# Optimization experiments

Measured on AMD Instinct MI355X. Metric: run time of the kernel, lower is better.

Reference implementation:

```python
import math
import jax, jax.numpy as jnp
import numpy as np

B, S, D = 2, 2048, 1024
N_HEADS, D_KV = 16, 64
INNER = N_HEADS * D_KV
NUM_BUCKETS = 32
MAX_DISTANCE = 128


def _relative_position_bucket(relative_position, num_buckets=NUM_BUCKETS, max_distance=MAX_DISTANCE):
    # bidirectional (encoder) variant
    nb = num_buckets // 2
    rel_buckets = (relative_position > 0).astype(jnp.int32) * nb
    rp = jnp.abs(relative_position)
    max_exact = nb // 2
    is_small = rp < max_exact
    rp_safe = jnp.maximum(rp, 1)  # avoid log(0); selected away by where
    rp_if_large = max_exact + (
        jnp.log(rp_safe.astype(jnp.float32) / max_exact)
        / math.log(max_distance / max_exact)
        * (nb - max_exact)
    ).astype(jnp.int32)
    rp_if_large = jnp.minimum(rp_if_large, nb - 1)
    return rel_buckets + jnp.where(is_small, rp, rp_if_large)


def compute_bias(rel_bias, q_len, k_len):
    ctx = jnp.arange(q_len)[:, None]
    mem = jnp.arange(k_len)[None, :]
    buckets = _relative_position_bucket(mem - ctx)  # [q_len, k_len]
    values = rel_bias[buckets]                      # [q_len, k_len, H]
    return jnp.transpose(values, (2, 0, 1))[None]   # [1, H, q_len, k_len]


def setup_inputs() -> dict:
    key = jax.random.key(0)
    ks = jax.random.split(key, 6)
    s = 1.0 / math.sqrt(D)
    return {
        "hidden_states": jax.random.normal(ks[0], (B, S, D), jnp.float32),
        "wq": jax.random.normal(ks[1], (D, INNER), jnp.float32) * s,
        "wk": jax.random.normal(ks[2], (D, INNER), jnp.float32) * s,
        "wv": jax.random.normal(ks[3], (D, INNER), jnp.float32) * s,
        "wo": jax.random.normal(ks[4], (INNER, D), jnp.float32) * s,
        "rel_bias": jax.random.normal(ks[5], (NUM_BUCKETS, N_HEADS), jnp.float32) * 0.1,
    }


def reference(hidden_states, wq, wk, wv, wo, rel_bias):
    b, s, _ = hidden_states.shape

    def shape(x):  # [b, s, inner] -> [b, h, s, d_kv]
        return x.reshape(b, s, N_HEADS, D_KV).transpose(0, 2, 1, 3)

    q = shape(hidden_states @ wq)  # note: T5 has NO 1/sqrt(d) scaling
    k = shape(hidden_states @ wk)
    v = shape(hidden_states @ wv)

    scores = jnp.einsum("bhqd,bhkd->bhqk", q, k)
    position_bias = compute_bias(rel_bias, s, s)
    scores = scores + position_bias
    attn = jax.nn.softmax(scores.astype(jnp.float32), axis=-1).astype(scores.dtype)

    out = jnp.einsum("bhqk,bhkd->bhqd", attn, v)
    out = out.transpose(0, 2, 1, 3).reshape(b, s, INNER)
    return out @ wo
```

## Files before the change

kernel.cpp:

```cpp
#include <hip/hip_runtime.h>
#include <hip/hip_bf16.h>

#define B_ 2
#define S_ 2048
#define D_ 1024
#define H_ 16
#define DKV_ 64
#define INNER_ 1024
#define M_ (B_*S_)

typedef unsigned short ushort_t;
typedef unsigned int u32;
typedef __bf16 bf16x8 __attribute__((ext_vector_type(8)));
typedef __bf16 bf16x4 __attribute__((ext_vector_type(4)));
typedef float f32x4 __attribute__((ext_vector_type(4)));

#define VMCNT0 asm volatile("s_waitcnt vmcnt(0)" ::: "memory")
#define LOG2E 1.4426950408889634f

__device__ __forceinline__ unsigned short f2bf(float f) {
    unsigned int u = __builtin_bit_cast(unsigned int, f);
    unsigned int r = (u + 0x7fffu + ((u >> 16) & 1u)) >> 16;
    return (unsigned short)r;
}

__device__ __forceinline__ void gload16(const ushort_t* g, ushort_t* l) {
    __builtin_amdgcn_global_load_lds(
        (const __attribute__((address_space(1))) u32*)g,
        (__attribute__((address_space(3))) u32*)l, 16, 0, 0);
}

__global__ __launch_bounds__(256) void prep_kernel(
        const float* __restrict__ hs,
        const float* __restrict__ s0, const float* __restrict__ s1,
        const float* __restrict__ s2, const float* __restrict__ s3,
        const float* __restrict__ rb,
        unsigned short* __restrict__ Abf,
        unsigned short* __restrict__ d0, unsigned short* __restrict__ d1,
        unsigned short* __restrict__ d2, unsigned short* __restrict__ d3,
        float* __restrict__ btab) {
    int bid = blockIdx.x, tid = threadIdx.x;
    if (bid < 4096) {
        int i = (bid * 256 + tid) * 4;
        float4 v = *(const float4*)&hs[i];
        ushort4 o;
        o.x = f2bf(v.x); o.y = f2bf(v.y); o.z = f2bf(v.z); o.w = f2bf(v.w);
        *(ushort4*)&Abf[i] = o;
    } else if (bid < 5120) {
        int t = bid - 4096;
        int z = t >> 8, rem = t & 255;
        int k0 = ((rem >> 4) & 15) * 64, n0 = (rem & 15) * 64;
        const float* srcs[4] = {s0, s1, s2, s3};
        unsigned short* dsts[4] = {d0, d1, d2, d3};
        const float* src = srcs[z];
        unsigned short* dst = dsts[z];
        __shared__ float tbuf[64][65];
        for (int i = tid; i < 4096; i += 256) {
            int r = i >> 6, c = i & 63;
            tbuf[r][c] = src[(k0 + r) * 1024 + n0 + c];
        }
        __syncthreads();
        for (int i = tid; i < 4096; i += 256) {
            int r = i >> 6, c = i & 63;
            dst[(n0 + r) * 1024 + k0 + c] = f2bf(tbuf[c][r]);
        }
    } else {
        #pragma unroll
        for (int j = 0; j < 4; ++j) {
            int idx = (bid - 5120) * 1024 + j * 256 + tid;
            int h = idx >> 12, pos = idx & 4095;
            int rel = pos - 2048;
            int bb = rel > 0 ? 16 : 0;
            int rp = rel < 0 ? -rel : rel;
            int bucket;
            if (rp < 8) bucket = bb + rp;
            else {
                int v = 8 + (int)(logf((float)rp * 0.125f) / 2.7725887f * 8.0f);
                bucket = bb + (v < 15 ? v : 15);
            }
            btab[idx] = rb[bucket * 16 + h] * LOG2E;
        }
    }
}

__global__ __launch_bounds__(256) void gemm_qkv(const ushort_t* __restrict__ A,
        const ushort_t* __restrict__ WQ, const ushort_t* __restrict__ WK, const ushort_t* __restrict__ WV,
        ushort_t* __restrict__ Qb, ushort_t* __restrict__ Kb, ushort_t* __restrict__ Vtb) {
    __shared__ alignas(16) ushort_t As[128][64];
    __shared__ alignas(16) ushort_t Bs[128][64];
    int tid = threadIdx.x, wid = tid >> 6, lane = tid & 63;
    int linear = blockIdx.x;
    int swz = (linear & 7) * 96 + (linear >> 3);
    int m0 = (swz / 24) * 128;
    int nblk = swz % 24;
    int sel = nblk >> 3;
    const ushort_t* Bt = sel == 0 ? WQ : (sel == 1 ? WK : WV);
    int n0 = (nblk & 7) * 128;
    int lr = lane & 15, lg = lane >> 4;
    int wm = (wid >> 1) * 64, wn = (wid & 1) * 64;
    int srow = tid >> 3, sp = tid & 7;
    int scol = (sp ^ (srow & 7)) * 8;
    int cR0 = (lg ^ (lr & 7)) * 8;
    int cR1 = ((4 + lg) ^ (lr & 7)) * 8;
    const ushort_t* Abase = A + (size_t)m0 * 1024 + scol;
    const ushort_t* Bbase = Bt + (size_t)n0 * 1024 + scol;
    f32x4 acc[4][4] = {};
    for (int kt = 0; kt < 1024; kt += 64) {
        #pragma unroll
        for (int j = 0; j < 4; ++j) {
            int row = j * 32 + srow;
            gload16(Abase + row * 1024 + kt, &As[0][0] + (j * 256 + tid) * 8);
            gload16(Bbase + row * 1024 + kt, &Bs[0][0] + (j * 256 + tid) * 8);
        }
        VMCNT0;
        __syncthreads();
        bf16x8 af[4][2], bfr[4][2];
        #pragma unroll
        for (int t = 0; t < 4; ++t) {
            af[t][0]  = *(const bf16x8*)&As[wm + t * 16 + lr][cR0];
            af[t][1]  = *(const bf16x8*)&As[wm + t * 16 + lr][cR1];
            bfr[t][0] = *(const bf16x8*)&Bs[wn + t * 16 + lr][cR0];
            bfr[t][1] = *(const bf16x8*)&Bs[wn + t * 16 + lr][cR1];
        }
        #pragma unroll
        for (int hh = 0; hh < 2; ++hh)
            #pragma unroll
            for (int i2 = 0; i2 < 4; ++i2)
                #pragma unroll
                for (int j2 = 0; j2 < 4; ++j2)
                    acc[i2][j2] = __builtin_amdgcn_mfma_f32_16x16x32_bf16(af[i2][hh], bfr[j2][hh], acc[i2][j2], 0, 0, 0);
        __syncthreads();
    }
    #pragma unroll
    for (int i2 = 0; i2 < 4; ++i2)
        #pragma unroll
        for (int j2 = 0; j2 < 4; ++j2) {
            int col = n0 + wn + j2 * 16 + lr;
            int hh = col >> 6, d = col & 63;
            if (sel < 2) {
                ushort_t* dst = sel == 0 ? Qb : Kb;
                #pragma unroll
                for (int r = 0; r < 4; ++r) {
                    int row = m0 + wm + i2 * 16 + lg * 4 + r;
                    int b = row >> 11, s = row & 2047;
                    dst[(((size_t)(b * H_ + hh) * S_ + s)) * DKV_ + d] = f2bf(acc[i2][j2][r]);
                }
            } else {
                int row0 = m0 + wm + i2 * 16 + lg * 4;
                int b = row0 >> 11, s0 = row0 & 2047;
                ushort4 sv;
                sv.x = f2bf(acc[i2][j2][0]); sv.y = f2bf(acc[i2][j2][1]);
                sv.z = f2bf(acc[i2][j2][2]); sv.w = f2bf(acc[i2][j2][3]);
                *(ushort4*)&Vtb[((size_t)(b * H_ + hh) * DKV_ + d) * S_ + s0] = sv;
            }
        }
}

__global__ __launch_bounds__(256) void gemm_out(const ushort_t* __restrict__ A,
                                                const ushort_t* __restrict__ Bt,
                                                float* __restrict__ C) {
    __shared__ alignas(16) ushort_t As[64][64];
    __shared__ alignas(16) ushort_t Bs[128][64];
    int tid = threadIdx.x, wid = tid >> 6, lane = tid & 63;
    int linear = blockIdx.x;
    int swz = (linear & 7) * 64 + (linear >> 3);
    int m0 = (swz >> 3) * 64, n0 = (swz & 7) * 128;
    int lr = lane & 15, lg = lane >> 4;
    int wn = wid * 32;
    int srow = tid >> 3, sp = tid & 7;
    int scol = (sp ^ (srow & 7)) * 8;
    int cR0 = (lg ^ (lr & 7)) * 8;
    int cR1 = ((4 + lg) ^ (lr & 7)) * 8;
    const ushort_t* Abase = A + (size_t)m0 * 1024 + scol;
    const ushort_t* Bbase = Bt + (size_t)n0 * 1024 + scol;
    f32x4 acc[4][2] = {};
    for (int kt = 0; kt < 1024; kt += 64) {
        #pragma unroll
        for (int j = 0; j < 2; ++j) {
            int row = j * 32 + srow;
            gload16(Abase + row * 1024 + kt, &As[0][0] + (j * 256 + tid) * 8);
        }
        #pragma unroll
        for (int j = 0; j < 4; ++j) {
            int row = j * 32 + srow;
            gload16(Bbase + row * 1024 + kt, &Bs[0][0] + (j * 256 + tid) * 8);
        }
        VMCNT0;
        __syncthreads();
        bf16x8 af[4][2], bfr[2][2];
        #pragma unroll
        for (int t = 0; t < 4; ++t) {
            af[t][0] = *(const bf16x8*)&As[t * 16 + lr][cR0];
            af[t][1] = *(const bf16x8*)&As[t * 16 + lr][cR1];
        }
        #pragma unroll
        for (int j = 0; j < 2; ++j) {
            bfr[j][0] = *(const bf16x8*)&Bs[wn + j * 16 + lr][cR0];
            bfr[j][1] = *(const bf16x8*)&Bs[wn + j * 16 + lr][cR1];
        }
        #pragma unroll
        for (int hh = 0; hh < 2; ++hh)
            #pragma unroll
            for (int i2 = 0; i2 < 4; ++i2)
                #pragma unroll
                for (int j2 = 0; j2 < 2; ++j2)
                    acc[i2][j2] = __builtin_amdgcn_mfma_f32_16x16x32_bf16(af[i2][hh], bfr[j2][hh], acc[i2][j2], 0, 0, 0);
        __syncthreads();
    }
    #pragma unroll
    for (int i2 = 0; i2 < 4; ++i2)
        #pragma unroll
        for (int j2 = 0; j2 < 2; ++j2)
            #pragma unroll
            for (int r = 0; r < 4; ++r)
                C[(size_t)(m0 + i2 * 16 + lg * 4 + r) * 1024 + n0 + wn + j2 * 16 + lr] = acc[i2][j2][r];
}

__global__ __launch_bounds__(256, 2) void flash_attn(const ushort_t* __restrict__ Q,
                                                     const ushort_t* __restrict__ Kg,
                                                     const ushort_t* __restrict__ Vt,
                                                     const float* __restrict__ bias_tab,
                                                     ushort_t* __restrict__ Out) {
    __shared__ alignas(16) ushort_t Ks[3][64][64];
    __shared__ alignas(16) ushort_t Ps[4][16][64];
    __shared__ float LbS[2176];
    int tid = threadIdx.x, wid = tid >> 6, lane = tid & 63;
    int linear = blockIdx.x;
    int swz = (linear & 7) * 64 + (linear >> 3);
    int bh = swz >> 4, qblk = swz & 15;
    int h = bh & 15, b = bh >> 4;
    int q0b = qblk * 128;
    int q0w = q0b + wid * 32;
    int lr = lane & 15, lg = lane >> 4;

    {
        const float* bsrc = bias_tab + h * 4096 + 2048 - q0b - 127;
        for (int i = tid; i < 2175; i += 256) LbS[i] = bsrc[i];
    }
    float cpos = bias_tab[h * 4096 + 4095];
    float cneg = bias_tab[h * 4096 + 0];

    const ushort_t* Qbase = Q + ((size_t)bh * S_ + q0w) * DKV_;
    bf16x8 qA0 = *(const bf16x8*)&Qbase[lr * DKV_ + lg * 8];
    bf16x8 qA1 = *(const bf16x8*)&Qbase[lr * DKV_ + 32 + lg * 8];
    bf16x8 qB0 = *(const bf16x8*)&Qbase[(16 + lr) * DKV_ + lg * 8];
    bf16x8 qB1 = *(const bf16x8*)&Qbase[(16 + lr) * DKV_ + 32 + lg * 8];

    int srow = tid >> 3, sp = tid & 7;
    int kc = (sp ^ (srow & 7)) * 8;
    const ushort_t* Ksrc = Kg + (size_t)bh * S_ * DKV_ + kc;
    const ushort_t* Vfrag = Vt + ((size_t)bh * DKV_ + lr) * S_ + lg * 8;
    int c0 = (lg ^ (lr & 7)) * 8;
    int c1 = ((4 + lg) ^ (lr & 7)) * 8;
    int pxor = (lr & 7) << 4;

    f32x4 oA[4] = {}, oB[4] = {};
    f32x4 lpA = {}, lpB = {};
    const int bbA = 127 - wid * 32 + 4 * lg - lr;
    const int bbB = bbA - 16;

    auto stageK = [&](int bi, int kt) {
        ushort_t* kb = &Ks[bi][0][0];
        gload16(Ksrc + (size_t)(kt + srow) * 64,      kb + tid * 8);
        gload16(Ksrc + (size_t)(kt + 32 + srow) * 64, kb + 2048 + tid * 8);
    };
    auto loadV = [&](int kt, bf16x8 (&v)[4][2]) {
        #pragma unroll
        for (int dt = 0; dt < 4; ++dt) {
            const ushort_t* vp = Vfrag + (size_t)dt * 16 * S_ + kt;
            v[dt][0] = *(const bf16x8*)vp;
            v[dt][1] = *(const bf16x8*)(vp + 32);
        }
    };
    auto qk = [&](int buf, f32x4* sA, f32x4* sB) {
        __builtin_amdgcn_s_setprio(1);
        #pragma unroll
        for (int nt = 0; nt < 4; ++nt) {
            bf16x8 kf0 = *(const bf16x8*)&Ks[buf][nt * 16 + lr][c0];
            bf16x8 kf1 = *(const bf16x8*)&Ks[buf][nt * 16 + lr][c1];
            sA[nt] = __builtin_amdgcn_mfma_f32_16x16x32_bf16(kf0, qA0, sA[nt], 0, 0, 0);
            sA[nt] = __builtin_amdgcn_mfma_f32_16x16x32_bf16(kf1, qA1, sA[nt], 0, 0, 0);
            sB[nt] = __builtin_amdgcn_mfma_f32_16x16x32_bf16(kf0, qB0, sB[nt], 0, 0, 0);
            sB[nt] = __builtin_amdgcn_mfma_f32_16x16x32_bf16(kf1, qB1, sB[nt], 0, 0, 0);
        }
        __builtin_amdgcn_s_setprio(0);
    };
    auto smpv = [&](f32x4 (&s)[4], f32x4& lp, f32x4 (&o)[4],
                    int bi, bool far, float cb, const bf16x8 (&vf)[4][2]) {
        float p[4][4];
        if (far) {
            #pragma unroll
            for (int nt = 0; nt < 4; ++nt)
                #pragma unroll
                for (int r = 0; r < 4; ++r)
                    p[nt][r] = __builtin_amdgcn_exp2f(fmaf(s[nt][r], LOG2E, cb));
        } else {
            #pragma unroll
            for (int nt = 0; nt < 4; ++nt)
                #pragma unroll
                for (int r = 0; r < 4; ++r)
                    p[nt][r] = __builtin_amdgcn_exp2f(fmaf(s[nt][r], LOG2E, LbS[bi + nt * 16 + r]));
        }
        char* pbase = (char*)&Ps[wid][lr][0];
        #pragma unroll
        for (int nt = 0; nt < 4; ++nt) {
            #pragma unroll
            for (int r = 0; r < 4; ++r) lp[r] += p[nt][r];
            bf16x4 pv;
            pv[0] = (__bf16)p[nt][0]; pv[1] = (__bf16)p[nt][1];
            pv[2] = (__bf16)p[nt][2]; pv[3] = (__bf16)p[nt][3];
            *(bf16x4*)(pbase + ((nt * 32 + lg * 8) ^ pxor)) = pv;
        }
        bf16x8 pf0 = *(const bf16x8*)(pbase + ((lg * 16) ^ pxor));
        bf16x8 pf1 = *(const bf16x8*)(pbase + ((64 + lg * 16) ^ pxor));
        __builtin_amdgcn_s_setprio(1);
        #pragma unroll
        for (int dt = 0; dt < 4; ++dt) {
            o[dt] = __builtin_amdgcn_mfma_f32_16x16x32_bf16(vf[dt][0], pf0, o[dt], 0, 0, 0);
            o[dt] = __builtin_amdgcn_mfma_f32_16x16x32_bf16(vf[dt][1], pf1, o[dt], 0, 0, 0);
        }
        __builtin_amdgcn_s_setprio(0);
    };

    bf16x8 vu[4][2], vn[4][2];
    f32x4 sCA[4] = {}, sCB[4] = {};

    stageK(0, 0);
    stageK(1, 64);
    stageK(2, 128);
    loadV(0, vu);
    asm volatile("s_waitcnt vmcnt(10) lgkmcnt(0)" ::: "memory");
    __builtin_amdgcn_s_barrier();
    __builtin_amdgcn_sched_barrier(0);
    qk(0, sCA, sCB);
    __builtin_amdgcn_s_barrier();
    __builtin_amdgcn_sched_barrier(0);

    #pragma unroll 2
    for (int t = 0; t < 32; ++t) {
        const int kt = t * 64;
        const bool even = (t & 1) == 0;
        bf16x8 (&vuse)[4][2] = even ? vu : vn;
        bf16x8 (&vnxt)[4][2] = even ? vn : vu;
        if (t <= 28) stageK(t % 3, kt + 192);
        if (t < 31) loadV(kt + 64, vnxt);
        __builtin_amdgcn_sched_barrier(0);
        f32x4 sNA[4] = {}, sNB[4] = {};
        if (t < 31) {
            int nb = (t + 1) % 3;
            qk(nb, sNA, sNB);
        }
        const bool far = (kt >= q0b + 256) || (kt + 64 <= q0b - 128);
        const float cb = (kt > q0b) ? cpos : cneg;
        smpv(sCA, lpA, oA, kt + bbA, far, cb, vuse);
        smpv(sCB, lpB, oB, kt + bbB, far, cb, vuse);
        #pragma unroll
        for (int nt = 0; nt < 4; ++nt) { sCA[nt] = sNA[nt]; sCB[nt] = sNB[nt]; }
        if (t < 31) {
            if (t <= 28) { asm volatile("s_waitcnt vmcnt(10)" ::: "memory"); }
            else         { asm volatile("s_waitcnt vmcnt(8)"  ::: "memory"); }
            __builtin_amdgcn_s_barrier();
            __builtin_amdgcn_sched_barrier(0);
        }
    }

    float lA = (lpA[0] + lpA[1]) + (lpA[2] + lpA[3]);
    lA += __shfl_xor(lA, 16); lA += __shfl_xor(lA, 32);
    float lB = (lpB[0] + lpB[1]) + (lpB[2] + lpB[3]);
    lB += __shfl_xor(lB, 16); lB += __shfl_xor(lB, 32);
    {
        float linv = 1.f / lA;
        char* pbase = (char*)&Ps[wid][lr][0];
        #pragma unroll
        for (int dt = 0; dt < 4; ++dt) {
            bf16x4 ov;
            ov[0] = (__bf16)(oA[dt][0] * linv); ov[1] = (__bf16)(oA[dt][1] * linv);
            ov[2] = (__bf16)(oA[dt][2] * linv); ov[3] = (__bf16)(oA[dt][3] * linv);
            *(bf16x4*)(pbase + ((dt * 32 + lg * 8) ^ pxor)) = ov;
        }
        int row = lane >> 2, seg = lane & 3;
        int rxor = (row & 7) << 4;
        char* rbase = (char*)&Ps[wid][row][0];
        uint4 v0 = *(uint4*)(rbase + ((seg * 32) ^ rxor));
        uint4 v1 = *(uint4*)(rbase + ((seg * 32 + 16) ^ rxor));
        ushort_t* dst = Out + (size_t)(b * S_ + q0w + row) * INNER_ + h * DKV_ + seg * 16;
        *(uint4*)&dst[0] = v0;
        *(uint4*)&dst[8] = v1;
    }
    {
        float linv = 1.f / lB;
        char* pbase = (char*)&Ps[wid][lr][0];
        #pragma unroll
        for (int dt = 0; dt < 4; ++dt) {
            bf16x4 ov;
            ov[0] = (__bf16)(oB[dt][0] * linv); ov[1] = (__bf16)(oB[dt][1] * linv);
            ov[2] = (__bf16)(oB[dt][2] * linv); ov[3] = (__bf16)(oB[dt][3] * linv);
            *(bf16x4*)(pbase + ((dt * 32 + lg * 8) ^ pxor)) = ov;
        }
        int row = lane >> 2, seg = lane & 3;
        int rxor = (row & 7) << 4;
        char* rbase = (char*)&Ps[wid][row][0];
        uint4 v0 = *(uint4*)(rbase + ((seg * 32) ^ rxor));
        uint4 v1 = *(uint4*)(rbase + ((seg * 32 + 16) ^ rxor));
        ushort_t* dst = Out + (size_t)(b * S_ + q0w + 16 + row) * INNER_ + h * DKV_ + seg * 16;
        *(uint4*)&dst[0] = v0;
        *(uint4*)&dst[8] = v1;
    }
}

extern "C" void kernel_launch(void* const* d_in, const int* in_sizes, int n_in,
                              void* d_out, int out_size, void* d_ws, size_t ws_size,
                              hipStream_t stream) {
    const float* hs = (const float*)d_in[0];
    const float* wq = (const float*)d_in[1];
    const float* wk = (const float*)d_in[2];
    const float* wv = (const float*)d_in[3];
    const float* wo = (const float*)d_in[4];
    const float* rb = (const float*)d_in[5];

    char* ws = (char*)d_ws;
    unsigned short* Abf = (unsigned short*)(ws);
    unsigned short* Wqt = (unsigned short*)(ws + (8u  << 20));
    unsigned short* Wkt = (unsigned short*)(ws + (10u << 20));
    unsigned short* Wvt = (unsigned short*)(ws + (12u << 20));
    unsigned short* Wot = (unsigned short*)(ws + (14u << 20));
    unsigned short* Qb  = (unsigned short*)(ws + (16u << 20));
    unsigned short* Kb  = (unsigned short*)(ws + (24u << 20));
    unsigned short* Vtb = (unsigned short*)(ws + (32u << 20));
    unsigned short* AOb = (unsigned short*)(ws + (40u << 20));
    float*          Btab = (float*)(ws + (48u << 20));

    prep_kernel<<<5184, 256, 0, stream>>>(hs, wq, wk, wv, wo, rb,
                                          Abf, Wqt, Wkt, Wvt, Wot, Btab);

    gemm_qkv<<<768, 256, 0, stream>>>(Abf, Wqt, Wkt, Wvt, Qb, Kb, Vtb);

    flash_attn<<<512, 256, 0, stream>>>(Qb, Kb, Vtb, Btab, AOb);

    gemm_out<<<512, 256, 0, stream>>>(AOb, Wot, (float*)d_out);
}
```

Baseline: 133.7 us.

## Feed P to PV MFMA directly from registers via 16x16x16 bf16 instruction

Replaces the LDS round-trip for the softmax probabilities (write P to shared memory, read back in K=32 layout) with the 16x16x16 bf16 MFMA, whose B-operand layout matches the QK accumulator layout, so P feeds the PV product straight from registers. V fragments are reloaded as 4-element chunks (16 narrower loads per tile instead of 8), and the vmcnt waits are adjusted to match. This removes LDS writes and reads plus their latency per tile, at the cost of twice as many MFMA issues for PV and more, smaller global loads. The old path is kept as a fallback when the builtin is unavailable.

```diff
diff --git a/kernel.cpp b/kernel.cpp
--- a/kernel.cpp
+++ b/kernel.cpp
@@ -13,6 +13,7 @@
 typedef unsigned int u32;
 typedef __bf16 bf16x8 __attribute__((ext_vector_type(8)));
 typedef __bf16 bf16x4 __attribute__((ext_vector_type(4)));
+typedef short s16x4 __attribute__((ext_vector_type(4)));
 typedef float f32x4 __attribute__((ext_vector_type(4)));
 
 #define VMCNT0 asm volatile("s_waitcnt vmcnt(0)" ::: "memory")
@@ -29,6 +30,14 @@
         (const __attribute__((address_space(1))) u32*)g,
         (__attribute__((address_space(3))) u32*)l, 16, 0, 0);
 }
+
+#if __has_builtin(__builtin_amdgcn_mfma_f32_16x16x16bf16_1k)
+#define HAVE_MFMA16 1
+__device__ __forceinline__ f32x4 mfma16(bf16x4 a, bf16x4 b, f32x4 c) {
+    return __builtin_amdgcn_mfma_f32_16x16x16bf16_1k(
+        __builtin_bit_cast(s16x4, a), __builtin_bit_cast(s16x4, b), c, 0, 0, 0);
+}
+#endif
 
 __global__ __launch_bounds__(256) void prep_kernel(
         const float* __restrict__ hs,
@@ -216,6 +225,7 @@
                 C[(size_t)(m0 + i2 * 16 + lg * 4 + r) * 1024 + n0 + wn + j2 * 16 + lr] = acc[i2][j2][r];
 }
 
+#ifdef HAVE_MFMA16
 __global__ __launch_bounds__(256, 2) void flash_attn(const ushort_t* __restrict__ Q,
                                                      const ushort_t* __restrict__ Kg,
                                                      const ushort_t* __restrict__ Vt,
@@ -249,7 +259,7 @@
     int srow = tid >> 3, sp = tid & 7;
     int kc = (sp ^ (srow & 7)) * 8;
     const ushort_t* Ksrc = Kg + (size_t)bh * S_ * DKV_ + kc;
-    const ushort_t* Vfrag = Vt + ((size_t)bh * DKV_ + lr) * S_ + lg * 8;
+    const ushort_t* VfragB = Vt + ((size_t)bh * DKV_ + lr) * S_ + lg * 4;
     int c0 = (lg ^ (lr & 7)) * 8;
     int c1 = ((4 + lg) ^ (lr & 7)) * 8;
     int pxor = (lr & 7) << 4;
@@ -264,13 +274,12 @@
         gload16(Ksrc + (size_t)(kt + srow) * 64,      kb + tid * 8);
         gload16(Ksrc + (size_t)(kt + 32 + srow) * 64, kb + 2048 + tid * 8);
     };
-    auto loadV = [&](int kt, bf16x8 (&v)[4][2]) {
-        #pragma unroll
-        for (int dt = 0; dt < 4; ++dt) {
-            const ushort_t* vp = Vfrag + (size_t)dt * 16 * S_ + kt;
-            v[dt][0] = *(const bf16x8*)vp;
-            v[dt][1] = *(const bf16x8*)(vp + 32);
-        }
+    auto loadV = [&](int kt, bf16x4 (&v)[4][4]) {
+        #pragma unroll
+        for (int dt = 0; dt < 4; ++dt)
+            #pragma unroll
+            for (int nt = 0; nt < 4; ++nt)
+                v[dt][nt] = *(const bf16x4*)(VfragB + (size_t)dt * 16 * S_ + kt + nt * 16);
     };
     auto qk = [&](int buf, f32x4* sA, f32x4* sB) {
         __builtin_amdgcn_s_setprio(1);
@@ -286,7 +295,7 @@
         __builtin_amdgcn_s_setprio(0);
     };
     auto smpv = [&](f32x4 (&s)[4], f32x4& lp, f32x4 (&o)[4],
-                    int bi, bool far, float cb, const bf16x8 (&vf)[4][2]) {
+                    int bi, bool far, float cb, const bf16x4 (&vf)[4][4]) {
         float p[4][4];
         if (far) {
             #pragma unroll
@@ -301,6 +310,189 @@
                 for (int r = 0; r < 4; ++r)
                     p[nt][r] = __builtin_amdgcn_exp2f(fmaf(s[nt][r], LOG2E, LbS[bi + nt * 16 + r]));
         }
+        bf16x4 pk[4];
+        #pragma unroll
+        for (int nt = 0; nt < 4; ++nt) {
+            #pragma unroll
+            for (int r = 0; r < 4; ++r) lp[r] += p[nt][r];
+            pk[nt][0] = (__bf16)p[nt][0]; pk[nt][1] = (__bf16)p[nt][1];
+            pk[nt][2] = (__bf16)p[nt][2]; pk[nt][3] = (__bf16)p[nt][3];
+        }
+        __builtin_amdgcn_s_setprio(1);
+        #pragma unroll
+        for (int dt = 0; dt < 4; ++dt)
+            #pragma unroll
+            for (int nt = 0; nt < 4; ++nt)
+                o[dt] = mfma16(vf[dt][nt], pk[nt], o[dt]);
+        __builtin_amdgcn_s_setprio(0);
+    };
+
+    bf16x4 vu[4][4], vn[4][4];
+    f32x4 sCA[4] = {}, sCB[4] = {};
+
+    stageK(0, 0);
+    stageK(1, 64);
+    stageK(2, 128);
+    loadV(0, vu);
+    asm volatile("s_waitcnt vmcnt(18) lgkmcnt(0)" ::: "memory");
+    __builtin_amdgcn_s_barrier();
+    __builtin_amdgcn_sched_barrier(0);
+    qk(0, sCA, sCB);
+    __builtin_amdgcn_s_barrier();
+    __builtin_amdgcn_sched_barrier(0);
+
+    #pragma unroll 2
+    for (int t = 0; t < 32; ++t) {
+        const int kt = t * 64;
+        const bool even = (t & 1) == 0;
+        bf16x4 (&vuse)[4][4] = even ? vu : vn;
+        bf16x4 (&vnxt)[4][4] = even ? vn : vu;
+        if (t <= 28) stageK(t % 3, kt + 192);
+        if (t < 31) loadV(kt + 64, vnxt);
+        __builtin_amdgcn_sched_barrier(0);
+        f32x4 sNA[4] = {}, sNB[4] = {};
+        if (t < 31) qk((t + 1) % 3, sNA, sNB);
+        const bool far = (kt >= q0b + 256) || (kt + 64 <= q0b - 128);
+        const float cb = (kt > q0b) ? cpos : cneg;
+        smpv(sCA, lpA, oA, kt + bbA, far, cb, vuse);
+        smpv(sCB, lpB, oB, kt + bbB, far, cb, vuse);
+        #pragma unroll
+        for (int nt = 0; nt < 4; ++nt) { sCA[nt] = sNA[nt]; sCB[nt] = sNB[nt]; }
+        if (t <= 28) {
+            asm volatile("s_waitcnt vmcnt(18)" ::: "memory");
+            __builtin_amdgcn_s_barrier();
+            __builtin_amdgcn_sched_barrier(0);
+        } else if (t == 29) {
+            asm volatile("s_waitcnt vmcnt(16)" ::: "memory");
+            __builtin_amdgcn_s_barrier();
+            __builtin_amdgcn_sched_barrier(0);
+        }
+    }
+
+    float lA = (lpA[0] + lpA[1]) + (lpA[2] + lpA[3]);
+    lA += __shfl_xor(lA, 16); lA += __shfl_xor(lA, 32);
+    float lB = (lpB[0] + lpB[1]) + (lpB[2] + lpB[3]);
+    lB += __shfl_xor(lB, 16); lB += __shfl_xor(lB, 32);
+    {
+        float linv = 1.f / lA;
+        char* pbase = (char*)&Ps[wid][lr][0];
+        #pragma unroll
+        for (int dt = 0; dt < 4; ++dt) {
+            bf16x4 ov;
+            ov[0] = (__bf16)(oA[dt][0] * linv); ov[1] = (__bf16)(oA[dt][1] * linv);
+            ov[2] = (__bf16)(oA[dt][2] * linv); ov[3] = (__bf16)(oA[dt][3] * linv);
+            *(bf16x4*)(pbase + ((dt * 32 + lg * 8) ^ pxor)) = ov;
+        }
+        int row = lane >> 2, seg = lane & 3;
+        int rxor = (row & 7) << 4;
+        char* rbase = (char*)&Ps[wid][row][0];
+        uint4 v0 = *(uint4*)(rbase + ((seg * 32) ^ rxor));
+        uint4 v1 = *(uint4*)(rbase + ((seg * 32 + 16) ^ rxor));
+        ushort_t* dst = Out + (size_t)(b * S_ + q0w + row) * INNER_ + h * DKV_ + seg * 16;
+        *(uint4*)&dst[0] = v0;
+        *(uint4*)&dst[8] = v1;
+    }
+    {
+        float linv = 1.f / lB;
+        char* pbase = (char*)&Ps[wid][lr][0];
+        #pragma unroll
+        for (int dt = 0; dt < 4; ++dt) {
+            bf16x4 ov;
+            ov[0] = (__bf16)(oB[dt][0] * linv); ov[1] = (__bf16)(oB[dt][1] * linv);
+            ov[2] = (__bf16)(oB[dt][2] * linv); ov[3] = (__bf16)(oB[dt][3] * linv);
+            *(bf16x4*)(pbase + ((dt * 32 + lg * 8) ^ pxor)) = ov;
+        }
+        int row = lane >> 2, seg = lane & 3;
+        int rxor = (row & 7) << 4;
+        char* rbase = (char*)&Ps[wid][row][0];
+        uint4 v0 = *(uint4*)(rbase + ((seg * 32) ^ rxor));
+        uint4 v1 = *(uint4*)(rbase + ((seg * 32 + 16) ^ rxor));
+        ushort_t* dst = Out + (size_t)(b * S_ + q0w + 16 + row) * INNER_ + h * DKV_ + seg * 16;
+        *(uint4*)&dst[0] = v0;
+        *(uint4*)&dst[8] = v1;
+    }
+}
+#else
+__global__ __launch_bounds__(256, 2) void flash_attn(const ushort_t* __restrict__ Q,
+                                                     const ushort_t* __restrict__ Kg,
+                                                     const ushort_t* __restrict__ Vt,
+                                                     const float* __restrict__ bias_tab,
+                                                     ushort_t* __restrict__ Out) {
+    __shared__ alignas(16) ushort_t Ks[3][64][64];
+    __shared__ alignas(16) ushort_t Ps[4][16][64];
+    __shared__ float LbS[2176];
+    int tid = threadIdx.x, wid = tid >> 6, lane = tid & 63;
+    int linear = blockIdx.x;
+    int swz = (linear & 7) * 64 + (linear >> 3);
+    int bh = swz >> 4, qblk = swz & 15;
+    int h = bh & 15, b = bh >> 4;
+    int q0b = qblk * 128;
+    int q0w = q0b + wid * 32;
+    int lr = lane & 15, lg = lane >> 4;
+    {
+        const float* bsrc = bias_tab + h * 4096 + 2048 - q0b - 127;
+        for (int i = tid; i < 2175; i += 256) LbS[i] = bsrc[i];
+    }
+    float cpos = bias_tab[h * 4096 + 4095];
+    float cneg = bias_tab[h * 4096 + 0];
+    const ushort_t* Qbase = Q + ((size_t)bh * S_ + q0w) * DKV_;
+    bf16x8 qA0 = *(const bf16x8*)&Qbase[lr * DKV_ + lg * 8];
+    bf16x8 qA1 = *(const bf16x8*)&Qbase[lr * DKV_ + 32 + lg * 8];
+    bf16x8 qB0 = *(const bf16x8*)&Qbase[(16 + lr) * DKV_ + lg * 8];
+    bf16x8 qB1 = *(const bf16x8*)&Qbase[(16 + lr) * DKV_ + 32 + lg * 8];
+    int srow = tid >> 3, sp = tid & 7;
+    int kc = (sp ^ (srow & 7)) * 8;
+    const ushort_t* Ksrc = Kg + (size_t)bh * S_ * DKV_ + kc;
+    const ushort_t* Vfrag = Vt + ((size_t)bh * DKV_ + lr) * S_ + lg * 8;
+    int c0 = (lg ^ (lr & 7)) * 8;
+    int c1 = ((4 + lg) ^ (lr & 7)) * 8;
+    int pxor = (lr & 7) << 4;
+    f32x4 oA[4] = {}, oB[4] = {};
+    f32x4 lpA = {}, lpB = {};
+    const int bbA = 127 - wid * 32 + 4 * lg - lr;
+    const int bbB = bbA - 16;
+    auto stageK = [&](int bi, int kt) {
+        ushort_t* kb = &Ks[bi][0][0];
+        gload16(Ksrc + (size_t)(kt + srow) * 64,      kb + tid * 8);
+        gload16(Ksrc + (size_t)(kt + 32 + srow) * 64, kb + 2048 + tid * 8);
+    };
+    auto loadV = [&](int kt, bf16x8 (&v)[4][2]) {
+        #pragma unroll
+        for (int dt = 0; dt < 4; ++dt) {
+            const ushort_t* vp = Vfrag + (size_t)dt * 16 * S_ + kt;
+            v[dt][0] = *(const bf16x8*)vp;
+            v[dt][1] = *(const bf16x8*)(vp + 32);
+        }
+    };
+    auto qk = [&](int buf, f32x4* sA, f32x4* sB) {
+        __builtin_amdgcn_s_setprio(1);
+        #pragma unroll
+        for (int nt = 0; nt < 4; ++nt) {
+            bf16x8 kf0 = *(const bf16x8*)&Ks[buf][nt * 16 + lr][c0];
+            bf16x8 kf1 = *(const bf16x8*)&Ks[buf][nt * 16 + lr][c1];
+            sA[nt] = __builtin_amdgcn_mfma_f32_16x16x32_bf16(kf0, qA0, sA[nt], 0, 0, 0);
+            sA[nt] = __builtin_amdgcn_mfma_f32_16x16x32_bf16(kf1, qA1, sA[nt], 0, 0, 0);
+            sB[nt] = __builtin_amdgcn_mfma_f32_16x16x32_bf16(kf0, qB0, sB[nt], 0, 0, 0);
+            sB[nt] = __builtin_amdgcn_mfma_f32_16x16x32_bf16(kf1, qB1, sB[nt], 0, 0, 0);
+        }
+        __builtin_amdgcn_s_setprio(0);
+    };
+    auto smpv = [&](f32x4 (&s)[4], f32x4& lp, f32x4 (&o)[4],
+                    int bi, bool far, float cb, const bf16x8 (&vf)[4][2]) {
+        float p[4][4];
+        if (far) {
+            #pragma unroll
+            for (int nt = 0; nt < 4; ++nt)
+                #pragma unroll
+                for (int r = 0; r < 4; ++r)
+                    p[nt][r] = __builtin_amdgcn_exp2f(fmaf(s[nt][r], LOG2E, cb));
+        } else {
+            #pragma unroll
+            for (int nt = 0; nt < 4; ++nt)
+                #pragma unroll
+                for (int r = 0; r < 4; ++r)
+                    p[nt][r] = __builtin_amdgcn_exp2f(fmaf(s[nt][r], LOG2E, LbS[bi + nt * 16 + r]));
+        }
         char* pbase = (char*)&Ps[wid][lr][0];
         #pragma unroll
         for (int nt = 0; nt < 4; ++nt) {
@@ -321,10 +513,8 @@
         }
         __builtin_amdgcn_s_setprio(0);
     };
-
     bf16x8 vu[4][2], vn[4][2];
     f32x4 sCA[4] = {}, sCB[4] = {};
-
     stageK(0, 0);
     stageK(1, 64);
     stageK(2, 128);
@@ -335,7 +525,6 @@
     qk(0, sCA, sCB);
     __builtin_amdgcn_s_barrier();
     __builtin_amdgcn_sched_barrier(0);
-
     #pragma unroll 2
     for (int t = 0; t < 32; ++t) {
         const int kt = t * 64;
@@ -346,10 +535,7 @@
         if (t < 31) loadV(kt + 64, vnxt);
         __builtin_amdgcn_sched_barrier(0);
         f32x4 sNA[4] = {}, sNB[4] = {};
-        if (t < 31) {
-            int nb = (t + 1) % 3;
-            qk(nb, sNA, sNB);
-        }
+        if (t < 31) qk((t + 1) % 3, sNA, sNB);
         const bool far = (kt >= q0b + 256) || (kt + 64 <= q0b - 128);
         const float cb = (kt > q0b) ? cpos : cneg;
         smpv(sCA, lpA, oA, kt + bbA, far, cb, vuse);
@@ -363,7 +549,6 @@
             __builtin_amdgcn_sched_barrier(0);
         }
     }
-
     float lA = (lpA[0] + lpA[1]) + (lpA[2] + lpA[3]);
     lA += __shfl_xor(lA, 16); lA += __shfl_xor(lA, 32);
     float lB = (lpB[0] + lpB[1]) + (lpB[2] + lpB[3]);
@@ -407,6 +592,7 @@
         *(uint4*)&dst[8] = v1;
     }
 }
+#endif
 
 extern "C" void kernel_launch(void* const* d_in, const int* in_sizes, int n_in,
                               void* d_out, int out_size, void* d_ws, size_t ws_size,
```

Result: slower. 186.1 us (+39.1%).
